# Kernel optimization log

Measured on AMD Instinct MI355X. Metric: run time of the kernel, lower is better.

Reference implementation:

```python
import jax, jax.numpy as jnp
import numpy as np

B, T, H, DEPTH = 16, 2048, 256, 3

def setup_inputs() -> dict:
    key = jax.random.key(0)
    ks = jax.random.split(key, 5)
    x = jax.random.normal(ks[0], (B, T, H), dtype=jnp.float32)
    seq_lens = jax.random.randint(ks[1], (B,), 1, T + 1, dtype=jnp.int32)
    s = 1.0 / np.sqrt(H)
    W_ih = jax.random.uniform(ks[2], (DEPTH, H, H), jnp.float32, -s, s)
    W_hh = jax.random.uniform(ks[3], (DEPTH, H, H), jnp.float32, -s, s)
    b = jax.random.uniform(ks[4], (DEPTH, H), jnp.float32, -s, s)
    return {"x": x, "seq_lens": seq_lens, "W_ih": W_ih, "W_hh": W_hh, "b": b}

def reference(x, seq_lens, W_ih, W_hh, b):
    # x: [B, T, D], stacked depth-3 single-state recurrent cells:
    #   h[t,k] = tanh(inp @ W_ih[k]^T + h[t-1,k] @ W_hh[k]^T + b[k])
    # where inp = x[t] for k==0 else h[t,k-1]; h[-1,k] = 0 (init_state).
    Bx, Tx, D = x.shape
    depth = W_ih.shape[0]
    h0 = jnp.zeros((depth, Bx, D), dtype=x.dtype)

    def step(h_prev, x_t):  # h_prev: [depth, B, H], x_t: [B, D]
        inp = x_t
        hs = []
        for k in range(depth):
            hk = jnp.tanh(inp @ W_ih[k].T + h_prev[k] @ W_hh[k].T + b[k])
            hs.append(hk)
            inp = hk
        h_new = jnp.stack(hs)  # [depth, B, H]
        return h_new, h_new

    _, ys = jax.lax.scan(step, h0, jnp.swapaxes(x, 0, 1))  # ys: [T, depth, B, H]
    out = jnp.transpose(ys, (2, 0, 1, 3))  # [B, T, depth, H]
    # positions past each sequence's length are never written (stay zero)
    mask = (jnp.arange(Tx)[None, :] < seq_lens[:, None])[:, :, None, None]
    return out * mask.astype(out.dtype)
```

## Files before the change

kernel.cpp:

```cpp
#include <hip/hip_runtime.h>
#include <stdint.h>


#define TT 2048
#define HH 256

typedef _Float16 h16x8 __attribute__((ext_vector_type(8)));
typedef float f32x4 __attribute__((ext_vector_type(4)));

__device__ __forceinline__ unsigned pkrtz(float a, float b) {
  return __builtin_bit_cast(unsigned, __builtin_amdgcn_cvt_pkrtz(a, b));
}

__device__ __forceinline__ float tanh_fast(float x) {
  float xm = fmaxf(x, -15.0f);
  float e = __builtin_amdgcn_exp2f(xm * -2.88539008177793f);
  float r = __builtin_amdgcn_rcpf(1.0f + e);
  return __builtin_fmaf(-2.0f * e, r, 1.0f);
}

__device__ __forceinline__ void spin_ge(int* p, int need) {
  while (__hip_atomic_load(p, __ATOMIC_ACQUIRE, __HIP_MEMORY_SCOPE_AGENT) < need)
    __builtin_amdgcn_s_sleep(2);
}

__global__ __launch_bounds__(512, 2)
void stacked_rnn(const float* __restrict__ x,
                 const int* __restrict__ seq_lens,
                 const float* __restrict__ Wih,
                 const float* __restrict__ Whh,
                 const float* __restrict__ bias,
                 float* __restrict__ out,
                 int* flags) {
  const int ks = blockIdx.x;
  const int tid = (int)threadIdx.x;
  const int w = tid >> 6;
  const int lane = tid & 63;
  const int q = lane >> 4;
  const int n = lane & 15;

  __shared__ unsigned short Bsm[2][8192];

  int* flag_up = flags + (ks - 1) * 64;
  int* flag_me = flags + ks * 64;

  h16x8 wf[2][16];
  {
    const float* wih_s = Wih + ks * (HH * HH);
    const float* whh_s = Whh + ks * (HH * HH);
#pragma unroll
    for (int mti = 0; mti < 2; ++mti) {
      const int fA = w * 32 + mti * 16 + n;
#pragma unroll
      for (int kt = 0; kt < 16; ++kt) {
        const int col = (kt & 7) * 32 + q * 8;
        const float* src = (kt < 8) ? (wih_s + fA * HH + col)
                                    : (whh_s + fA * HH + col);
        float4 a0 = ((const float4*)src)[0];
        float4 a1 = ((const float4*)src)[1];
        h16x8 f;
        f[0] = (_Float16)a0.x; f[1] = (_Float16)a0.y;
        f[2] = (_Float16)a0.z; f[3] = (_Float16)a0.w;
        f[4] = (_Float16)a1.x; f[5] = (_Float16)a1.y;
        f[6] = (_Float16)a1.z; f[7] = (_Float16)a1.w;
        wf[mti][kt] = f;
      }
    }
  }

  f32x4 biasv[2];
#pragma unroll
  for (int mti = 0; mti < 2; ++mti)
#pragma unroll
    for (int r = 0; r < 4; ++r)
      biasv[mti][r] = bias[ks * HH + w * 32 + mti * 16 + q * 4 + r];

  const int sl = seq_lens[n];

  const int rdE = (q * 16 + (n ^ q)) * 8;
  const int rdO = (q * 16 + (n ^ q ^ 4)) * 8;

  int hofs[2];
#pragma unroll
  for (int mti = 0; mti < 2; ++mti) {
    const int u = (8 + w) * 4 + mti * 2 + (q >> 1);
    hofs[mti] = (u * 16 + (n ^ (u & 7))) * 8 + (q & 1) * 4;
  }

  const int n_l = tid >> 5;
  const int k8  = tid & 31;
  const int u_l = (k8 >> 2) * 4 + (k8 & 3);
  const int ldst = (u_l * 16 + (n_l ^ (u_l & 7))) * 8;

  const float* src_base;
  int src_stride;
  if (ks == 0) {
    src_base = x + ((n_l * TT) << 8) + (k8 << 3);
    src_stride = HH;
  } else {
    src_base = out + (((n_l * TT) * 3 + (ks - 1)) << 8) + (k8 << 3);
    src_stride = 3 * HH;
  }

  for (int i = tid; i < 4096; i += 512) Bsm[0][4096 + i] = 0;
  if (ks > 0 && tid == 0) spin_ge(flag_up, 18);
  __syncthreads();

  {
    float4 c0 = ((const float4*)src_base)[0];
    float4 c1 = ((const float4*)src_base)[1];
    *(uint4*)&Bsm[0][ldst] = make_uint4(pkrtz(c0.x, c0.y), pkrtz(c0.z, c0.w),
                                        pkrtz(c1.x, c1.y), pkrtz(c1.z, c1.w));
  }
  float4 pfB0 = ((const float4*)(src_base + src_stride))[0];
  float4 pfB1 = ((const float4*)(src_base + src_stride))[1];
  const float* src_pf = src_base + 2 * src_stride;
  __syncthreads();

  float* outp = out + ((n * TT) * 3 + ks) * HH + w * 32 + q * 4;

  for (int t = 0; t < TT; ++t) {
    unsigned short* Bp = Bsm[t & 1];
    unsigned short* Bq = Bsm[(t & 1) ^ 1];

    if ((t & 7) == 0 && t > 0 && ks < 2 && tid == 0)
      __hip_atomic_store(flag_me, t, __ATOMIC_RELEASE,
                         __HIP_MEMORY_SCOPE_AGENT);
    if ((t & 15) == 0 && t > 0 && ks > 0) {
      if (tid == 0) {
        int need = t + 18;
        if (need > TT) need = TT;
        spin_ge(flag_up, need);
      }
      __syncthreads();
    }

    float4 pfA0, pfA1;
    const bool more2 = (t + 2 < TT);
    if (more2) {
      pfA0 = ((const float4*)src_pf)[0];
      pfA1 = ((const float4*)src_pf)[1];
    }
    src_pf += src_stride;

    f32x4 acc[2] = {biasv[0], biasv[1]};
#pragma unroll
    for (int kt = 0; kt < 16; ++kt) {
      const int ofs = ((kt & 1) ? rdO : rdE) + kt * 512;
      h16x8 bf = *(const h16x8*)&Bp[ofs];
      acc[0] = __builtin_amdgcn_mfma_f32_16x16x32_f16(wf[0][kt], bf, acc[0], 0, 0, 0);
      acc[1] = __builtin_amdgcn_mfma_f32_16x16x32_f16(wf[1][kt], bf, acc[1], 0, 0, 0);
    }

    const bool live = (t < sl);
    uint2 hpk[2];
#pragma unroll
    for (int mti = 0; mti < 2; ++mti) {
      float h0 = tanh_fast(acc[mti][0]);
      float h1 = tanh_fast(acc[mti][1]);
      float h2 = tanh_fast(acc[mti][2]);
      float h3 = tanh_fast(acc[mti][3]);
      hpk[mti].x = pkrtz(h0, h1);
      hpk[mti].y = pkrtz(h2, h3);
      float4 od;
      od.x = live ? h0 : 0.0f;
      od.y = live ? h1 : 0.0f;
      od.z = live ? h2 : 0.0f;
      od.w = live ? h3 : 0.0f;
      *(float4*)(outp + mti * 16) = od;
    }
    outp += 3 * HH;

    if (t + 1 < TT) {
      *(uint4*)&Bq[ldst] = make_uint4(pkrtz(pfB0.x, pfB0.y), pkrtz(pfB0.z, pfB0.w),
                                      pkrtz(pfB1.x, pfB1.y), pkrtz(pfB1.z, pfB1.w));
      *(uint2*)&Bq[hofs[0]] = hpk[0];
      *(uint2*)&Bq[hofs[1]] = hpk[1];
      if (more2) { pfB0 = pfA0; pfB1 = pfA1; }
    }

    __syncthreads();
  }

  if (ks < 2 && tid == 0)
    __hip_atomic_store(flag_me, TT, __ATOMIC_RELEASE, __HIP_MEMORY_SCOPE_AGENT);
}

extern "C" void kernel_launch(void* const* d_in, const int* in_sizes, int n_in,
                              void* d_out, int out_size, void* d_ws, size_t ws_size,
                              hipStream_t stream) {
  (void)in_sizes; (void)n_in; (void)out_size; (void)ws_size;
  const float* x   = (const float*)d_in[0];
  const int*   sl  = (const int*)d_in[1];
  const float* wih = (const float*)d_in[2];
  const float* whh = (const float*)d_in[3];
  const float* b   = (const float*)d_in[4];

  (void)hipMemsetAsync(d_ws, 0, 1024, stream);
  hipLaunchKernelGGL(stacked_rnn, dim3(3), dim3(512), 0, stream,
                     x, sl, wih, whh, b, (float*)d_out, (int*)d_ws);
}
```

Before: 2.303 ms.

## Split input projection into separate feeder blocks streaming through a ring buffer

Each layer's input projection (W_ih @ input + bias) moves off the serial recurrent path into two dedicated feeder blocks per layer. The feeders write precomputed pre-activations into a 64-step global ring buffer and signal progress with per-chunk flags. The recurrent blocks then do only the W_hh half of the MFMA work per timestep, halving the serial critical path. In exchange it adds 6 extra blocks, global ring traffic, and more inter-block spin-wait synchronisation, with some risk of ordering or visibility bugs.

```diff
diff --git a/kernel.cpp b/kernel.cpp
--- a/kernel.cpp
+++ b/kernel.cpp
@@ -4,6 +4,8 @@
 
 #define TT 2048
 #define HH 256
+#define RING 64
+#define NCH (TT / 8)
 
 typedef _Float16 h16x8 __attribute__((ext_vector_type(8)));
 typedef float f32x4 __attribute__((ext_vector_type(4)));
@@ -31,159 +33,192 @@
                  const float* __restrict__ Whh,
                  const float* __restrict__ bias,
                  float* __restrict__ out,
-                 int* flags) {
-  const int ks = blockIdx.x;
+                 int* __restrict__ flags,
+                 float* __restrict__ ring) {
+  const int bid = blockIdx.x;
   const int tid = (int)threadIdx.x;
   const int w = tid >> 6;
   const int lane = tid & 63;
   const int q = lane >> 4;
   const int n = lane & 15;
 
-  __shared__ unsigned short Bsm[2][8192];
-
-  int* flag_up = flags + (ks - 1) * 64;
-  int* flag_me = flags + ks * 64;
-
-  h16x8 wf[2][16];
-  {
-    const float* wih_s = Wih + ks * (HH * HH);
-    const float* whh_s = Whh + ks * (HH * HH);
-#pragma unroll
-    for (int mti = 0; mti < 2; ++mti) {
-      const int fA = w * 32 + mti * 16 + n;
-#pragma unroll
-      for (int kt = 0; kt < 16; ++kt) {
-        const int col = (kt & 7) * 32 + q * 8;
-        const float* src = (kt < 8) ? (wih_s + fA * HH + col)
-                                    : (whh_s + fA * HH + col);
-        float4 a0 = ((const float4*)src)[0];
-        float4 a1 = ((const float4*)src)[1];
-        h16x8 f;
-        f[0] = (_Float16)a0.x; f[1] = (_Float16)a0.y;
-        f[2] = (_Float16)a0.z; f[3] = (_Float16)a0.w;
-        f[4] = (_Float16)a1.x; f[5] = (_Float16)a1.y;
-        f[6] = (_Float16)a1.z; f[7] = (_Float16)a1.w;
-        wf[mti][kt] = f;
-      }
+  const bool is_rec = (bid < 3);
+  const int ks = is_rec ? bid : ((bid - 3) >> 1);
+
+  __shared__ unsigned short Bsm[2][4096];
+
+  const float* Wsel = (is_rec ? Whh : Wih) + ks * HH * HH;
+  h16x8 wf[2][8];
+#pragma unroll
+  for (int mti = 0; mti < 2; ++mti) {
+    const int fA = w * 32 + mti * 16 + n;
+#pragma unroll
+    for (int kt = 0; kt < 8; ++kt) {
+      const float* src = Wsel + fA * HH + kt * 32 + q * 8;
+      float4 a0 = ((const float4*)src)[0];
+      float4 a1 = ((const float4*)src)[1];
+      h16x8 f;
+      f[0] = (_Float16)a0.x; f[1] = (_Float16)a0.y;
+      f[2] = (_Float16)a0.z; f[3] = (_Float16)a0.w;
+      f[4] = (_Float16)a1.x; f[5] = (_Float16)a1.y;
+      f[6] = (_Float16)a1.z; f[7] = (_Float16)a1.w;
+      wf[mti][kt] = f;
     }
   }
-
-  f32x4 biasv[2];
-#pragma unroll
-  for (int mti = 0; mti < 2; ++mti)
-#pragma unroll
-    for (int r = 0; r < 4; ++r)
-      biasv[mti][r] = bias[ks * HH + w * 32 + mti * 16 + q * 4 + r];
-
-  const int sl = seq_lens[n];
 
   const int rdE = (q * 16 + (n ^ q)) * 8;
   const int rdO = (q * 16 + (n ^ q ^ 4)) * 8;
 
-  int hofs[2];
-#pragma unroll
-  for (int mti = 0; mti < 2; ++mti) {
-    const int u = (8 + w) * 4 + mti * 2 + (q >> 1);
-    hofs[mti] = (u * 16 + (n ^ (u & 7))) * 8 + (q & 1) * 4;
+  float* ringk = ring + ks * (RING * 4096);
+  const int prow = n * 256 + w * 32 + q * 4;
+
+  int* rec_flag_me = flags + ks * 16;
+  int* feed_base = flags + 64 + ks * NCH;
+
+  if (is_rec) {
+    const int sl = seq_lens[n];
+    int hofs[2];
+#pragma unroll
+    for (int mti = 0; mti < 2; ++mti) {
+      const int u = w * 4 + mti * 2 + (q >> 1);
+      hofs[mti] = (u * 16 + (n ^ (u & 7))) * 8 + (q & 1) * 4;
+    }
+    for (int i = tid; i < 4096; i += 512) Bsm[0][i] = 0;
+
+    if (tid == 0) { spin_ge(feed_base + 0, 1); spin_ge(feed_base + 1, 2); }
+    __syncthreads();
+
+    f32x4 pf0 = *(const f32x4*)(ringk + prow);
+    f32x4 pf1 = *(const f32x4*)(ringk + prow + 16);
+
+    float* outp = out + ((n * TT) * 3 + ks) * HH + w * 32 + q * 4;
+
+    for (int t = 0; t < TT; ++t) {
+      if ((t & 7) == 0 && t > 0) {
+        if (tid == 0) {
+          __hip_atomic_store(rec_flag_me, t, __ATOMIC_RELEASE,
+                             __HIP_MEMORY_SCOPE_AGENT);
+          const int c = t >> 3;
+          spin_ge(feed_base + c, c + 1);
+          if (c + 1 < NCH) spin_ge(feed_base + c + 1, c + 2);
+        }
+        __syncthreads();
+      }
+
+      f32x4 pA0, pA1;
+      if (t + 1 < TT) {
+        const float* pb = ringk + ((t + 1) & (RING - 1)) * 4096 + prow;
+        pA0 = *(const f32x4*)pb;
+        pA1 = *(const f32x4*)(pb + 16);
+      }
+
+      const unsigned short* Bp = Bsm[t & 1];
+      f32x4 acc0 = pf0, acc1 = pf1;
+#pragma unroll
+      for (int kt = 0; kt < 8; ++kt) {
+        h16x8 bf = *(const h16x8*)&Bp[((kt & 1) ? rdO : rdE) + kt * 512];
+        acc0 = __builtin_amdgcn_mfma_f32_16x16x32_f16(wf[0][kt], bf, acc0, 0, 0, 0);
+        acc1 = __builtin_amdgcn_mfma_f32_16x16x32_f16(wf[1][kt], bf, acc1, 0, 0, 0);
+      }
+
+      const bool live = (t < sl);
+      uint2 hpk[2];
+      f32x4 accs[2] = {acc0, acc1};
+#pragma unroll
+      for (int mti = 0; mti < 2; ++mti) {
+        float h0 = tanh_fast(accs[mti][0]);
+        float h1 = tanh_fast(accs[mti][1]);
+        float h2 = tanh_fast(accs[mti][2]);
+        float h3 = tanh_fast(accs[mti][3]);
+        hpk[mti].x = pkrtz(h0, h1);
+        hpk[mti].y = pkrtz(h2, h3);
+        float4 od;
+        od.x = live ? h0 : 0.0f;
+        od.y = live ? h1 : 0.0f;
+        od.z = live ? h2 : 0.0f;
+        od.w = live ? h3 : 0.0f;
+        *(float4*)(outp + mti * 16) = od;
+      }
+      outp += 3 * HH;
+
+      if (t + 1 < TT) {
+        unsigned short* Bq = Bsm[(t & 1) ^ 1];
+        *(uint2*)&Bq[hofs[0]] = hpk[0];
+        *(uint2*)&Bq[hofs[1]] = hpk[1];
+        pf0 = pA0; pf1 = pA1;
+      }
+      __syncthreads();
+    }
+    if (tid == 0)
+      __hip_atomic_store(rec_flag_me, TT, __ATOMIC_RELEASE,
+                         __HIP_MEMORY_SCOPE_AGENT);
+  } else {
+    const int fid = (bid - 3) & 1;
+
+    f32x4 biasv[2];
+#pragma unroll
+    for (int mti = 0; mti < 2; ++mti)
+#pragma unroll
+      for (int r = 0; r < 4; ++r)
+        biasv[mti][r] = bias[ks * HH + w * 32 + mti * 16 + q * 4 + r];
+
+    const int n_l = tid >> 5, k8 = tid & 31;
+    const int u_l = (k8 >> 2) * 4 + (k8 & 3);
+    const int ldst = (u_l * 16 + (n_l ^ (u_l & 7))) * 8;
+    const float* src_base;
+    int sstr;
+    if (ks == 0) { src_base = x + ((n_l * TT) << 8) + (k8 << 3); sstr = HH; }
+    else { src_base = out + (((n_l * TT) * 3 + (ks - 1)) << 8) + (k8 << 3); sstr = 3 * HH; }
+
+    int* rec_flag_up = flags + (ks - 1) * 16;
+
+    for (int c = fid; c < NCH; c += 2) {
+      const int t0 = c * 8;
+      if (tid == 0) {
+        if (ks > 0) spin_ge(rec_flag_up, t0 + 8);
+        if (t0 >= RING) spin_ge(rec_flag_me, t0 - (RING - 8));
+      }
+      __syncthreads();
+
+      {
+        const float* s = src_base + t0 * sstr;
+        float4 c0 = ((const float4*)s)[0], c1 = ((const float4*)s)[1];
+        *(uint4*)&Bsm[0][ldst] = make_uint4(pkrtz(c0.x, c0.y), pkrtz(c0.z, c0.w),
+                                            pkrtz(c1.x, c1.y), pkrtz(c1.z, c1.w));
+      }
+      __syncthreads();
+
+      for (int s = 0; s < 8; ++s) {
+        const int t = t0 + s;
+        float4 i0, i1;
+        if (s < 7) {
+          const float* sp = src_base + (t + 1) * sstr;
+          i0 = ((const float4*)sp)[0];
+          i1 = ((const float4*)sp)[1];
+        }
+        const unsigned short* Bp = Bsm[s & 1];
+        f32x4 acc0 = biasv[0], acc1 = biasv[1];
+#pragma unroll
+        for (int kt = 0; kt < 8; ++kt) {
+          h16x8 bf = *(const h16x8*)&Bp[((kt & 1) ? rdO : rdE) + kt * 512];
+          acc0 = __builtin_amdgcn_mfma_f32_16x16x32_f16(wf[0][kt], bf, acc0, 0, 0, 0);
+          acc1 = __builtin_amdgcn_mfma_f32_16x16x32_f16(wf[1][kt], bf, acc1, 0, 0, 0);
+        }
+        float* pd = ringk + (t & (RING - 1)) * 4096 + prow;
+        *(f32x4*)pd = acc0;
+        *(f32x4*)(pd + 16) = acc1;
+        if (s < 7) {
+          unsigned short* Bq = Bsm[(s & 1) ^ 1];
+          *(uint4*)&Bq[ldst] = make_uint4(pkrtz(i0.x, i0.y), pkrtz(i0.z, i0.w),
+                                          pkrtz(i1.x, i1.y), pkrtz(i1.z, i1.w));
+        }
+        __syncthreads();
+      }
+      if (tid == 0)
+        __hip_atomic_store(feed_base + c, c + 1, __ATOMIC_RELEASE,
+                           __HIP_MEMORY_SCOPE_AGENT);
+    }
   }
-
-  const int n_l = tid >> 5;
-  const int k8  = tid & 31;
-  const int u_l = (k8 >> 2) * 4 + (k8 & 3);
-  const int ldst = (u_l * 16 + (n_l ^ (u_l & 7))) * 8;
-
-  const float* src_base;
-  int src_stride;
-  if (ks == 0) {
-    src_base = x + ((n_l * TT) << 8) + (k8 << 3);
-    src_stride = HH;
-  } else {
-    src_base = out + (((n_l * TT) * 3 + (ks - 1)) << 8) + (k8 << 3);
-    src_stride = 3 * HH;
-  }
-
-  for (int i = tid; i < 4096; i += 512) Bsm[0][4096 + i] = 0;
-  if (ks > 0 && tid == 0) spin_ge(flag_up, 18);
-  __syncthreads();
-
-  {
-    float4 c0 = ((const float4*)src_base)[0];
-    float4 c1 = ((const float4*)src_base)[1];
-    *(uint4*)&Bsm[0][ldst] = make_uint4(pkrtz(c0.x, c0.y), pkrtz(c0.z, c0.w),
-                                        pkrtz(c1.x, c1.y), pkrtz(c1.z, c1.w));
-  }
-  float4 pfB0 = ((const float4*)(src_base + src_stride))[0];
-  float4 pfB1 = ((const float4*)(src_base + src_stride))[1];
-  const float* src_pf = src_base + 2 * src_stride;
-  __syncthreads();
-
-  float* outp = out + ((n * TT) * 3 + ks) * HH + w * 32 + q * 4;
-
-  for (int t = 0; t < TT; ++t) {
-    unsigned short* Bp = Bsm[t & 1];
-    unsigned short* Bq = Bsm[(t & 1) ^ 1];
-
-    if ((t & 7) == 0 && t > 0 && ks < 2 && tid == 0)
-      __hip_atomic_store(flag_me, t, __ATOMIC_RELEASE,
-                         __HIP_MEMORY_SCOPE_AGENT);
-    if ((t & 15) == 0 && t > 0 && ks > 0) {
-      if (tid == 0) {
-        int need = t + 18;
-        if (need > TT) need = TT;
-        spin_ge(flag_up, need);
-      }
-      __syncthreads();
-    }
-
-    float4 pfA0, pfA1;
-    const bool more2 = (t + 2 < TT);
-    if (more2) {
-      pfA0 = ((const float4*)src_pf)[0];
-      pfA1 = ((const float4*)src_pf)[1];
-    }
-    src_pf += src_stride;
-
-    f32x4 acc[2] = {biasv[0], biasv[1]};
-#pragma unroll
-    for (int kt = 0; kt < 16; ++kt) {
-      const int ofs = ((kt & 1) ? rdO : rdE) + kt * 512;
-      h16x8 bf = *(const h16x8*)&Bp[ofs];
-      acc[0] = __builtin_amdgcn_mfma_f32_16x16x32_f16(wf[0][kt], bf, acc[0], 0, 0, 0);
-      acc[1] = __builtin_amdgcn_mfma_f32_16x16x32_f16(wf[1][kt], bf, acc[1], 0, 0, 0);
-    }
-
-    const bool live = (t < sl);
-    uint2 hpk[2];
-#pragma unroll
-    for (int mti = 0; mti < 2; ++mti) {
-      float h0 = tanh_fast(acc[mti][0]);
-      float h1 = tanh_fast(acc[mti][1]);
-      float h2 = tanh_fast(acc[mti][2]);
-      float h3 = tanh_fast(acc[mti][3]);
-      hpk[mti].x = pkrtz(h0, h1);
-      hpk[mti].y = pkrtz(h2, h3);
-      float4 od;
-      od.x = live ? h0 : 0.0f;
-      od.y = live ? h1 : 0.0f;
-      od.z = live ? h2 : 0.0f;
-      od.w = live ? h3 : 0.0f;
-      *(float4*)(outp + mti * 16) = od;
-    }
-    outp += 3 * HH;
-
-    if (t + 1 < TT) {
-      *(uint4*)&Bq[ldst] = make_uint4(pkrtz(pfB0.x, pfB0.y), pkrtz(pfB0.z, pfB0.w),
-                                      pkrtz(pfB1.x, pfB1.y), pkrtz(pfB1.z, pfB1.w));
-      *(uint2*)&Bq[hofs[0]] = hpk[0];
-      *(uint2*)&Bq[hofs[1]] = hpk[1];
-      if (more2) { pfB0 = pfA0; pfB1 = pfA1; }
-    }
-
-    __syncthreads();
-  }
-
-  if (ks < 2 && tid == 0)
-    __hip_atomic_store(flag_me, TT, __ATOMIC_RELEASE, __HIP_MEMORY_SCOPE_AGENT);
 }
 
 extern "C" void kernel_launch(void* const* d_in, const int* in_sizes, int n_in,
@@ -196,7 +231,8 @@
   const float* whh = (const float*)d_in[3];
   const float* b   = (const float*)d_in[4];
 
-  (void)hipMemsetAsync(d_ws, 0, 1024, stream);
-  hipLaunchKernelGGL(stacked_rnn, dim3(3), dim3(512), 0, stream,
-                     x, sl, wih, whh, b, (float*)d_out, (int*)d_ws);
-}
+  (void)hipMemsetAsync(d_ws, 0, 4096, stream);
+  float* ring = (float*)((char*)d_ws + 8192);
+  hipLaunchKernelGGL(stacked_rnn, dim3(9), dim3(512), 0, stream,
+                     x, sl, wih, whh, b, (float*)d_out, (int*)d_ws, ring);
+}
```

After: 2.807 ms. 1.22x slower.
